# Kernel optimization log

Hardware: AMD Instinct MI355X
Metric: run time of the kernel (lower is better)

## Reference

```python
import jax, jax.numpy as jnp
import numpy as np

EPS = 1e-6

def _grad_magnitude(x):
    # x: [B, 1, D, H, W]. Valid 3x3x3 conv with shift-subtract kernels:
    # kernel_w differences along D, kernel_d along H, kernel_h along W.
    g_w = x[:, :, 2:, 1:-1, 1:-1] - x[:, :, :-2, 1:-1, 1:-1]
    g_d = x[:, :, 1:-1, 2:, 1:-1] - x[:, :, 1:-1, :-2, 1:-1]
    g_h = x[:, :, 1:-1, 1:-1, 2:] - x[:, :, 1:-1, 1:-1, :-2]
    mag = jnp.sqrt(g_w * g_w + g_d * g_d + g_h * g_h + EPS)
    # replicate-pad back to original spatial size
    return jnp.pad(mag, ((0, 0), (0, 0), (1, 1), (1, 1), (1, 1)), mode='edge')

def setup_inputs() -> dict:
    key = jax.random.key(0)
    k1, k2 = jax.random.split(key)
    shape = (1, 1, 256, 256, 256)
    x1 = jax.random.normal(k1, shape, dtype=jnp.float32)
    x2 = jax.random.normal(k2, shape, dtype=jnp.float32)
    return {"x1": x1, "x2": x2}

def reference(x1, x2):
    g1 = _grad_magnitude(x1)
    g2 = _grad_magnitude(x2)
    return jnp.mean(jnp.abs(g1 - g2))
```

## Files before the change

kernel.cpp:

```cpp
#include <hip/hip_runtime.h>


#define D_CHUNK 8

__global__ __launch_bounds__(256, 4) void grad_loss_kernel(const float* __restrict__ xf1,
                                                           const float* __restrict__ xf2,
                                                           double* __restrict__ acc) {
    const float4* __restrict__ x1 = (const float4*)xf1;
    const float4* __restrict__ x2 = (const float4*)xf2;

    const int tid  = threadIdx.x;
    const int lane = tid & 63;
    const int wid  = tid >> 6;

    const int orig = blockIdx.x;
    const int wg   = (orig & 7) * 256 + (orig >> 3);
    const int htile = wg & 63;
    const int dchk  = wg >> 6;

    const int  r    = 1 + htile * 4 + wid;
    const bool live = (r <= 254);
    const int  rc   = (r <= 255) ? r : 255;
    const int  rm   = r - 1;
    const int  rp   = (r + 1 <= 255) ? (r + 1) : 255;

    const int iU = rm * 64 + lane;
    const int iC = rc * 64 + lane;
    const int iV = rp * 64 + lane;

    const int d0 = 1 + dchk * D_CHUNK;

    const float ww0 = (lane == 0)  ? 0.0f : 1.0f;
    const float ww1 = (lane == 0)  ? 2.0f : 1.0f;
    const float ww2 = (lane == 63) ? 2.0f : 1.0f;
    const float ww3 = (lane == 63) ? 0.0f : 1.0f;
    const float whf = (r == 1 || r == 254) ? 2.0f : 1.0f;

    float4 a1  = x1[(d0 - 1) * 16384 + iC];
    float4 a2  = x2[(d0 - 1) * 16384 + iC];
    float4 bU1 = x1[d0 * 16384 + iU];
    float4 bC1 = x1[d0 * 16384 + iC];
    float4 bV1 = x1[d0 * 16384 + iV];
    float4 bU2 = x2[d0 * 16384 + iU];
    float4 bC2 = x2[d0 * 16384 + iC];
    float4 bV2 = x2[d0 * 16384 + iV];
    float4 cU1 = x1[(d0 + 1) * 16384 + iU];
    float4 cC1 = x1[(d0 + 1) * 16384 + iC];
    float4 cV1 = x1[(d0 + 1) * 16384 + iV];
    float4 cU2 = x2[(d0 + 1) * 16384 + iU];
    float4 cC2 = x2[(d0 + 1) * 16384 + iC];
    float4 cV2 = x2[(d0 + 1) * 16384 + iV];

    float val = 0.0f;

    #pragma unroll 2
    for (int i = 0; i < D_CHUNK; ++i) {
        const int d  = d0 + i;
        const int dn = (d + 2 <= 255) ? (d + 2) : 255;
        const int off = dn * 16384;

        float4 qU1 = x1[off + iU];
        float4 qC1 = x1[off + iC];
        float4 qV1 = x1[off + iV];
        float4 qU2 = x2[off + iU];
        float4 qC2 = x2[off + iC];
        float4 qV2 = x2[off + iV];

        if (live && d <= 254) {
            float l1 = __shfl_up(bC1.w, 1, 64);
            float r1 = __shfl_down(bC1.x, 1, 64);
            float l2 = __shfl_up(bC2.w, 1, 64);
            float r2 = __shfl_down(bC2.x, 1, 64);

            float gw, gd, gh;
            gw = cC1.x - a1.x; gd = bV1.x - bU1.x; gh = bC1.y - l1;
            float m10 = __builtin_amdgcn_sqrtf(gw * gw + gd * gd + gh * gh + 1e-6f);
            gw = cC1.y - a1.y; gd = bV1.y - bU1.y; gh = bC1.z - bC1.x;
            float m11 = __builtin_amdgcn_sqrtf(gw * gw + gd * gd + gh * gh + 1e-6f);
            gw = cC1.z - a1.z; gd = bV1.z - bU1.z; gh = bC1.w - bC1.y;
            float m12 = __builtin_amdgcn_sqrtf(gw * gw + gd * gd + gh * gh + 1e-6f);
            gw = cC1.w - a1.w; gd = bV1.w - bU1.w; gh = r1 - bC1.z;
            float m13 = __builtin_amdgcn_sqrtf(gw * gw + gd * gd + gh * gh + 1e-6f);

            gw = cC2.x - a2.x; gd = bV2.x - bU2.x; gh = bC2.y - l2;
            float m20 = __builtin_amdgcn_sqrtf(gw * gw + gd * gd + gh * gh + 1e-6f);
            gw = cC2.y - a2.y; gd = bV2.y - bU2.y; gh = bC2.z - bC2.x;
            float m21 = __builtin_amdgcn_sqrtf(gw * gw + gd * gd + gh * gh + 1e-6f);
            gw = cC2.z - a2.z; gd = bV2.z - bU2.z; gh = bC2.w - bC2.y;
            float m22 = __builtin_amdgcn_sqrtf(gw * gw + gd * gd + gh * gh + 1e-6f);
            gw = cC2.w - a2.w; gd = bV2.w - bU2.w; gh = r2 - bC2.z;
            float m23 = __builtin_amdgcn_sqrtf(gw * gw + gd * gd + gh * gh + 1e-6f);

            float inner = ww0 * fabsf(m10 - m20)
                        + ww1 * fabsf(m11 - m21)
                        + ww2 * fabsf(m12 - m22)
                        + ww3 * fabsf(m13 - m23);

            const float wdf = (d == 1 || d == 254) ? 2.0f : 1.0f;
            val += wdf * whf * inner;
        }

        a1 = bC1; bU1 = cU1; bC1 = cC1; bV1 = cV1; cU1 = qU1; cC1 = qC1; cV1 = qV1;
        a2 = bC2; bU2 = cU2; bC2 = cC2; bV2 = cV2; cU2 = qU2; cC2 = qC2; cV2 = qV2;
    }

    for (int off = 32; off > 0; off >>= 1)
        val += __shfl_down(val, off, 64);

    __shared__ float smem[4];
    if (lane == 0) smem[wid] = val;
    __syncthreads();

    if (wid == 0) {
        float s = (lane < 4) ? smem[lane] : 0.0f;
        s += __shfl_down(s, 2, 64);
        s += __shfl_down(s, 1, 64);
        if (lane == 0)
            atomicAdd(&acc[blockIdx.x & 255], (double)s);
    }
}

__global__ void finalize_kernel(const double* __restrict__ acc, float* __restrict__ out) {
    double v = acc[threadIdx.x];
    for (int off = 32; off > 0; off >>= 1)
        v += __shfl_down(v, off, 64);

    __shared__ double smem[4];
    const int lid = threadIdx.x & 63;
    const int wid = threadIdx.x >> 6;
    if (lid == 0) smem[wid] = v;
    __syncthreads();

    if (threadIdx.x == 0) {
        double s = smem[0] + smem[1] + smem[2] + smem[3];
        out[0] = (float)(s / 16777216.0);
    }
}

extern "C" void kernel_launch(void* const* d_in, const int* in_sizes, int n_in,
                              void* d_out, int out_size, void* d_ws, size_t ws_size,
                              hipStream_t stream) {
    const float* x1 = (const float*)d_in[0];
    const float* x2 = (const float*)d_in[1];
    float* out = (float*)d_out;
    double* acc = (double*)d_ws;

    hipMemsetAsync(d_ws, 0, 256 * sizeof(double), stream);
    grad_loss_kernel<<<64 * 32, 256, 0, stream>>>(x1, x2, acc);
    finalize_kernel<<<1, 256, 0, stream>>>(acc, out);
}
```

Measured before the change: 154.3 us.

## Compute two H rows per wave to reuse shared neighbor row loads

Each wavefront now handles two adjacent H rows, loading four row vectors per D slice per input instead of three per row. This cuts redundant global/cache loads of the overlapping neighbor rows. The grid is halved, launch bounds drop to 3 blocks per CU, and the D loop is fully unrolled. The cost is higher register use and fewer resident waves, which could hurt latency hiding.

```diff
diff --git a/kernel.cpp b/kernel.cpp
--- a/kernel.cpp
+++ b/kernel.cpp
@@ -3,7 +3,42 @@
 
 #define D_CHUNK 8
 
-__global__ __launch_bounds__(256, 4) void grad_loss_kernel(const float* __restrict__ xf1,
+__device__ __forceinline__ float row_term(float4 bU1, float4 bC1, float4 bV1,
+                                          float4 a1, float4 c1,
+                                          float4 bU2, float4 bC2, float4 bV2,
+                                          float4 a2, float4 c2,
+                                          float ww0, float ww1, float ww2, float ww3) {
+    float l1 = __shfl_up(bC1.w, 1, 64);
+    float r1 = __shfl_down(bC1.x, 1, 64);
+    float l2 = __shfl_up(bC2.w, 1, 64);
+    float r2 = __shfl_down(bC2.x, 1, 64);
+
+    float gw, gd, gh;
+    gw = c1.x - a1.x; gd = bV1.x - bU1.x; gh = bC1.y - l1;
+    float m10 = __builtin_amdgcn_sqrtf(gw * gw + gd * gd + gh * gh + 1e-6f);
+    gw = c1.y - a1.y; gd = bV1.y - bU1.y; gh = bC1.z - bC1.x;
+    float m11 = __builtin_amdgcn_sqrtf(gw * gw + gd * gd + gh * gh + 1e-6f);
+    gw = c1.z - a1.z; gd = bV1.z - bU1.z; gh = bC1.w - bC1.y;
+    float m12 = __builtin_amdgcn_sqrtf(gw * gw + gd * gd + gh * gh + 1e-6f);
+    gw = c1.w - a1.w; gd = bV1.w - bU1.w; gh = r1 - bC1.z;
+    float m13 = __builtin_amdgcn_sqrtf(gw * gw + gd * gd + gh * gh + 1e-6f);
+
+    gw = c2.x - a2.x; gd = bV2.x - bU2.x; gh = bC2.y - l2;
+    float m20 = __builtin_amdgcn_sqrtf(gw * gw + gd * gd + gh * gh + 1e-6f);
+    gw = c2.y - a2.y; gd = bV2.y - bU2.y; gh = bC2.z - bC2.x;
+    float m21 = __builtin_amdgcn_sqrtf(gw * gw + gd * gd + gh * gh + 1e-6f);
+    gw = c2.z - a2.z; gd = bV2.z - bU2.z; gh = bC2.w - bC2.y;
+    float m22 = __builtin_amdgcn_sqrtf(gw * gw + gd * gd + gh * gh + 1e-6f);
+    gw = c2.w - a2.w; gd = bV2.w - bU2.w; gh = r2 - bC2.z;
+    float m23 = __builtin_amdgcn_sqrtf(gw * gw + gd * gd + gh * gh + 1e-6f);
+
+    return ww0 * fabsf(m10 - m20)
+         + ww1 * fabsf(m11 - m21)
+         + ww2 * fabsf(m12 - m22)
+         + ww3 * fabsf(m13 - m23);
+}
+
+__global__ __launch_bounds__(256, 3) void grad_loss_kernel(const float* __restrict__ xf1,
                                                            const float* __restrict__ xf2,
                                                            double* __restrict__ acc) {
     const float4* __restrict__ x1 = (const float4*)xf1;
@@ -14,19 +49,23 @@
     const int wid  = tid >> 6;
 
     const int orig = blockIdx.x;
-    const int wg   = (orig & 7) * 256 + (orig >> 3);
-    const int htile = wg & 63;
-    const int dchk  = wg >> 6;
+    const int wg   = (orig & 7) * 128 + (orig >> 3);
+    const int htile = wg & 31;
+    const int dchk  = wg >> 5;
 
-    const int  r    = 1 + htile * 4 + wid;
-    const bool live = (r <= 254);
-    const int  rc   = (r <= 255) ? r : 255;
-    const int  rm   = r - 1;
-    const int  rp   = (r + 1 <= 255) ? (r + 1) : 255;
+    const int r0 = 1 + htile * 8 + wid * 2;
+    const bool live0 = (r0 <= 254);
+    const bool live1 = (r0 + 1 <= 254);
 
-    const int iU = rm * 64 + lane;
-    const int iC = rc * 64 + lane;
-    const int iV = rp * 64 + lane;
+    const int rm  = r0 - 1;
+    const int rc0 = (r0 <= 255) ? r0 : 255;
+    const int rc1 = (r0 + 1 <= 255) ? (r0 + 1) : 255;
+    const int rp  = (r0 + 2 <= 255) ? (r0 + 2) : 255;
+
+    const int iM = rm  * 64 + lane;
+    const int i0 = rc0 * 64 + lane;
+    const int i1 = rc1 * 64 + lane;
+    const int iP = rp  * 64 + lane;
 
     const int d0 = 1 + dchk * D_CHUNK;
 
@@ -34,74 +73,68 @@
     const float ww1 = (lane == 0)  ? 2.0f : 1.0f;
     const float ww2 = (lane == 63) ? 2.0f : 1.0f;
     const float ww3 = (lane == 63) ? 0.0f : 1.0f;
-    const float whf = (r == 1 || r == 254) ? 2.0f : 1.0f;
+    const float whf0 = (r0 == 1 || r0 == 254) ? 2.0f : 1.0f;
+    const float whf1 = (r0 + 1 == 1 || r0 + 1 == 254) ? 2.0f : 1.0f;
 
-    float4 a1  = x1[(d0 - 1) * 16384 + iC];
-    float4 a2  = x2[(d0 - 1) * 16384 + iC];
-    float4 bU1 = x1[d0 * 16384 + iU];
-    float4 bC1 = x1[d0 * 16384 + iC];
-    float4 bV1 = x1[d0 * 16384 + iV];
-    float4 bU2 = x2[d0 * 16384 + iU];
-    float4 bC2 = x2[d0 * 16384 + iC];
-    float4 bV2 = x2[d0 * 16384 + iV];
-    float4 cU1 = x1[(d0 + 1) * 16384 + iU];
-    float4 cC1 = x1[(d0 + 1) * 16384 + iC];
-    float4 cV1 = x1[(d0 + 1) * 16384 + iV];
-    float4 cU2 = x2[(d0 + 1) * 16384 + iU];
-    float4 cC2 = x2[(d0 + 1) * 16384 + iC];
-    float4 cV2 = x2[(d0 + 1) * 16384 + iV];
+    float4 pA01 = x1[(d0 - 1) * 16384 + i0];
+    float4 pA11 = x1[(d0 - 1) * 16384 + i1];
+    float4 pA02 = x2[(d0 - 1) * 16384 + i0];
+    float4 pA12 = x2[(d0 - 1) * 16384 + i1];
+
+    float4 pBm1 = x1[d0 * 16384 + iM];
+    float4 pB01 = x1[d0 * 16384 + i0];
+    float4 pB11 = x1[d0 * 16384 + i1];
+    float4 pBp1 = x1[d0 * 16384 + iP];
+    float4 pBm2 = x2[d0 * 16384 + iM];
+    float4 pB02 = x2[d0 * 16384 + i0];
+    float4 pB12 = x2[d0 * 16384 + i1];
+    float4 pBp2 = x2[d0 * 16384 + iP];
+
+    float4 pCm1 = x1[(d0 + 1) * 16384 + iM];
+    float4 pC01 = x1[(d0 + 1) * 16384 + i0];
+    float4 pC11 = x1[(d0 + 1) * 16384 + i1];
+    float4 pCp1 = x1[(d0 + 1) * 16384 + iP];
+    float4 pCm2 = x2[(d0 + 1) * 16384 + iM];
+    float4 pC02 = x2[(d0 + 1) * 16384 + i0];
+    float4 pC12 = x2[(d0 + 1) * 16384 + i1];
+    float4 pCp2 = x2[(d0 + 1) * 16384 + iP];
 
     float val = 0.0f;
 
-    #pragma unroll 2
+    #pragma unroll
     for (int i = 0; i < D_CHUNK; ++i) {
         const int d  = d0 + i;
         const int dn = (d + 2 <= 255) ? (d + 2) : 255;
         const int off = dn * 16384;
 
-        float4 qU1 = x1[off + iU];
-        float4 qC1 = x1[off + iC];
-        float4 qV1 = x1[off + iV];
-        float4 qU2 = x2[off + iU];
-        float4 qC2 = x2[off + iC];
-        float4 qV2 = x2[off + iV];
+        float4 qm1 = x1[off + iM];
+        float4 q01 = x1[off + i0];
+        float4 q11 = x1[off + i1];
+        float4 qp1 = x1[off + iP];
+        float4 qm2 = x2[off + iM];
+        float4 q02 = x2[off + i0];
+        float4 q12 = x2[off + i1];
+        float4 qp2 = x2[off + iP];
 
-        if (live && d <= 254) {
-            float l1 = __shfl_up(bC1.w, 1, 64);
-            float r1 = __shfl_down(bC1.x, 1, 64);
-            float l2 = __shfl_up(bC2.w, 1, 64);
-            float r2 = __shfl_down(bC2.x, 1, 64);
-
-            float gw, gd, gh;
-            gw = cC1.x - a1.x; gd = bV1.x - bU1.x; gh = bC1.y - l1;
-            float m10 = __builtin_amdgcn_sqrtf(gw * gw + gd * gd + gh * gh + 1e-6f);
-            gw = cC1.y - a1.y; gd = bV1.y - bU1.y; gh = bC1.z - bC1.x;
-            float m11 = __builtin_amdgcn_sqrtf(gw * gw + gd * gd + gh * gh + 1e-6f);
-            gw = cC1.z - a1.z; gd = bV1.z - bU1.z; gh = bC1.w - bC1.y;
-            float m12 = __builtin_amdgcn_sqrtf(gw * gw + gd * gd + gh * gh + 1e-6f);
-            gw = cC1.w - a1.w; gd = bV1.w - bU1.w; gh = r1 - bC1.z;
-            float m13 = __builtin_amdgcn_sqrtf(gw * gw + gd * gd + gh * gh + 1e-6f);
-
-            gw = cC2.x - a2.x; gd = bV2.x - bU2.x; gh = bC2.y - l2;
-            float m20 = __builtin_amdgcn_sqrtf(gw * gw + gd * gd + gh * gh + 1e-6f);
-            gw = cC2.y - a2.y; gd = bV2.y - bU2.y; gh = bC2.z - bC2.x;
-            float m21 = __builtin_amdgcn_sqrtf(gw * gw + gd * gd + gh * gh + 1e-6f);
-            gw = cC2.z - a2.z; gd = bV2.z - bU2.z; gh = bC2.w - bC2.y;
-            float m22 = __builtin_amdgcn_sqrtf(gw * gw + gd * gd + gh * gh + 1e-6f);
-            gw = cC2.w - a2.w; gd = bV2.w - bU2.w; gh = r2 - bC2.z;
-            float m23 = __builtin_amdgcn_sqrtf(gw * gw + gd * gd + gh * gh + 1e-6f);
-
-            float inner = ww0 * fabsf(m10 - m20)
-                        + ww1 * fabsf(m11 - m21)
-                        + ww2 * fabsf(m12 - m22)
-                        + ww3 * fabsf(m13 - m23);
-
+        if (d <= 254) {
             const float wdf = (d == 1 || d == 254) ? 2.0f : 1.0f;
-            val += wdf * whf * inner;
+            float t = 0.0f;
+            if (live0)
+                t += whf0 * row_term(pBm1, pB01, pB11, pA01, pC01,
+                                     pBm2, pB02, pB12, pA02, pC02,
+                                     ww0, ww1, ww2, ww3);
+            if (live1)
+                t += whf1 * row_term(pB01, pB11, pBp1, pA11, pC11,
+                                     pB02, pB12, pBp2, pA12, pC12,
+                                     ww0, ww1, ww2, ww3);
+            val += wdf * t;
         }
 
-        a1 = bC1; bU1 = cU1; bC1 = cC1; bV1 = cV1; cU1 = qU1; cC1 = qC1; cV1 = qV1;
-        a2 = bC2; bU2 = cU2; bC2 = cC2; bV2 = cV2; cU2 = qU2; cC2 = qC2; cV2 = qV2;
+        pA01 = pB01; pA11 = pB11; pA02 = pB02; pA12 = pB12;
+        pBm1 = pCm1; pB01 = pC01; pB11 = pC11; pBp1 = pCp1;
+        pBm2 = pCm2; pB02 = pC02; pB12 = pC12; pBp2 = pCp2;
+        pCm1 = qm1;  pC01 = q01;  pC11 = q11;  pCp1 = qp1;
+        pCm2 = qm2;  pC02 = q02;  pC12 = q12;  pCp2 = qp2;
     }
 
     for (int off = 32; off > 0; off >>= 1)
@@ -146,6 +179,6 @@
     double* acc = (double*)d_ws;
 
     hipMemsetAsync(d_ws, 0, 256 * sizeof(double), stream);
-    grad_loss_kernel<<<64 * 32, 256, 0, stream>>>(x1, x2, acc);
+    grad_loss_kernel<<<32 * 32, 256, 0, stream>>>(x1, x2, acc);
     finalize_kernel<<<1, 256, 0, stream>>>(acc, out);
 }
```

After: 150.7 us. -2.3%, faster.
